# Kernel optimization log

Measured on AMD Instinct MI355X. Metric: run time of the kernel, lower is better.

The kernel has to match this reference:

```python
import jax, jax.numpy as jnp
import numpy as np

DECAY = 0.99
EPS = 1e-05


def setup_inputs() -> dict:
    key = jax.random.key(0)
    k1, k2, k3 = jax.random.split(key, 3)
    inputs = jax.random.normal(k1, (16, 32, 32, 128), dtype=jnp.float32)
    cluster_mean = jax.random.normal(k2, (128, 10000), dtype=jnp.float32)
    cluster_sum = jax.random.normal(k3, (128, 10000), dtype=jnp.float32)
    cluster_size = jnp.zeros((10000,), dtype=jnp.float32)
    return {"inputs": inputs, "cluster_mean": cluster_mean,
            "cluster_sum": cluster_sum, "cluster_size": cluster_size}


def reference(inputs, cluster_mean, cluster_sum, cluster_size):
    embed_dim, n_embed = cluster_mean.shape
    samples = inputs.reshape(-1, embed_dim)                      # [N, E]

    # squared-euclidean distance to each codebook entry: [N, K]
    dist = (jnp.sum(samples ** 2, axis=1, keepdims=True)
            - 2.0 * samples @ cluster_mean
            + jnp.sum(cluster_mean ** 2, axis=0, keepdims=True))
    cluster_index = jnp.argmin(dist, axis=1)                     # [N] int

    # EMA statistics (segment-sum instead of materializing [N, K] one-hot)
    counts = jax.ops.segment_sum(jnp.ones_like(cluster_index, dtype=samples.dtype),
                                 cluster_index, num_segments=n_embed)      # [K]
    sums = jax.ops.segment_sum(samples, cluster_index, num_segments=n_embed).T  # [E, K]

    new_cluster_size = cluster_size * DECAY + counts * (1.0 - DECAY)
    new_cluster_sum = cluster_sum * DECAY + sums * (1.0 - DECAY)

    n_sample = jnp.sum(new_cluster_size)
    smoothed = (new_cluster_size + EPS) * n_sample / (n_sample + n_embed * EPS)
    new_cluster_mean = new_cluster_sum / smoothed                # [E, K]

    idx_grid = cluster_index.reshape(inputs.shape[:-1])          # [B, H, W]
    quantize = new_cluster_mean.T[idx_grid]                      # [B, H, W, E]

    e_loss = jnp.mean((inputs - jax.lax.stop_gradient(quantize)) ** 2)
    outputs = inputs + jax.lax.stop_gradient(quantize - inputs)  # straight-through
    return outputs, 0.25 * e_loss, new_cluster_mean, new_cluster_size, new_cluster_sum
```

## Files before the change

kernel.cpp:

```cpp
#include <hip/hip_runtime.h>

#define NS 16384
#define ED 128
#define KC 10000
#define KP 10240
#define EKTOT (ED*KC)

#define O_OUT  0
#define O_LOSS (NS*ED)
#define O_MEAN (O_LOSS+1)
#define O_SIZE (O_MEAN+EKTOT)
#define O_SUM  (O_SIZE+KC)

#define WB_BEST  0u
#define WB_CNORM 131072u
#define WB_IDX   172032u
#define WB_CNT   237568u
#define WB_NS    278528u
#define WB_XH    294912u
#define WB_XL    4489216u
#define WB_MH    8683520u
#define WB_ML    11304960u

typedef _Float16 f16;
typedef _Float16 f16x8 __attribute__((ext_vector_type(8)));
typedef _Float16 f16x4 __attribute__((ext_vector_type(4)));
typedef float f32x4 __attribute__((ext_vector_type(4)));

constexpr float DECAY = 0.99f;
constexpr float OMD   = 0.01f;
constexpr float EPSV  = 1e-5f;

__global__ void k_prep(const float* __restrict__ X, const float* __restrict__ M,
                       const float* __restrict__ CZ,
                       f16* __restrict__ Xh, f16* __restrict__ Xl,
                       f16* __restrict__ Mh, f16* __restrict__ Ml,
                       float* __restrict__ cnorm, float* __restrict__ cnt,
                       unsigned long long* __restrict__ best,
                       float* __restrict__ out, float* __restrict__ ns_cz) {
    const int b = blockIdx.x, t = threadIdx.x;
    if (b < 2048) {
        int i = (b * 256 + t) * 4;
        float4 v = *(const float4*)(X + i);
        f16x4 h, l;
        h[0] = (f16)v.x; l[0] = (f16)(v.x - (float)h[0]);
        h[1] = (f16)v.y; l[1] = (f16)(v.y - (float)h[1]);
        h[2] = (f16)v.z; l[2] = (f16)(v.z - (float)h[2]);
        h[3] = (f16)v.w; l[3] = (f16)(v.w - (float)h[3]);
        *(f16x4*)(Xh + i) = h;
        *(f16x4*)(Xl + i) = l;
        if (t < 160) {
            int f4 = b * 160 + t;
            if (f4 * 4 < EKTOT) *(float4*)(out + f4 * 4) = make_float4(0.f, 0.f, 0.f, 0.f);
        }
    } else if (b < 2088) {
        int k = (b - 2048) * 256 + t;
        float s = __builtin_inff();
        if (k < KC) {
            s = 0.f;
            #pragma unroll
            for (int c = 0; c < 16; ++c) {
                f16x8 h, l;
                #pragma unroll
                for (int j = 0; j < 8; ++j) {
                    float m = M[(size_t)(c * 8 + j) * KC + k];
                    s = fmaf(m, m, s);
                    h[j] = (f16)m;
                    l[j] = (f16)(m - (float)h[j]);
                }
                *(f16x8*)(Mh + (size_t)k * ED + c * 8) = h;
                *(f16x8*)(Ml + (size_t)k * ED + c * 8) = l;
            }
        } else {
            f16x8 z = {0, 0, 0, 0, 0, 0, 0, 0};
            #pragma unroll
            for (int c = 0; c < 16; ++c) {
                *(f16x8*)(Mh + (size_t)k * ED + c * 8) = z;
                *(f16x8*)(Ml + (size_t)k * ED + c * 8) = z;
            }
        }
        cnorm[k] = s;
        cnt[k] = 0.f;
        for (int i = k; i < NS; i += 40 * 256) best[i] = ~0ull;
    } else {
        __shared__ float red[256];
        float s = 0.f;
        for (int i = t; i < KC; i += 256) s += CZ[i];
        red[t] = s;
        __syncthreads();
        for (int st = 128; st > 0; st >>= 1) {
            if (t < st) red[t] += red[t + st];
            __syncthreads();
        }
        if (t == 0) { *ns_cz = red[0]; out[O_LOSS] = 0.f; }
    }
}

__launch_bounds__(256, 4)
__global__ void k_assign(const f16* __restrict__ Xh, const f16* __restrict__ Xl,
                         const f16* __restrict__ Mh, const f16* __restrict__ Ml,
                         const float* __restrict__ cnorm,
                         unsigned long long* __restrict__ best) {
    __shared__ f16 As[128 * 64];
    __shared__ f16 Bs[128 * 64];

    const int c0 = blockIdx.x * 128;
    const int n0 = blockIdx.y * 128;
    const int t = threadIdx.x, w = t >> 6, l = t & 63;
    const int wr = w >> 1, wc = w & 1;
    const int lg = l >> 4, li = l & 15;

    f32x4 acc[4][4];
    #pragma unroll
    for (int i = 0; i < 4; ++i)
        #pragma unroll
        for (int j = 0; j < 4; ++j) acc[i][j] = (f32x4)0.f;

    const f16* Ap[6] = {Xh, Xh, Xl, Xh, Xh, Xl};
    const f16* Bp[6] = {Mh, Ml, Mh, Mh, Ml, Mh};

    for (int st = 0; st < 6; ++st) {
        const int hh = st < 3 ? 0 : 1;
        const bool loadA = (st != 1) && (st != 4);
        const f16* A = Ap[st];
        const f16* B = Bp[st];
        __syncthreads();
        #pragma unroll
        for (int it = 0; it < 4; ++it) {
            int f = it * 256 + t;
            int row = f >> 3, seg = f & 7;
            int segS = seg ^ (row & 7);
            const f16* gb = B + (size_t)(c0 + row) * ED + hh * 64 + segS * 8;
            f16* lb = Bs + (it * 256 + w * 64) * 8;
            __builtin_amdgcn_global_load_lds(
                (const __attribute__((address_space(1))) unsigned int*)gb,
                (__attribute__((address_space(3))) unsigned int*)lb, 16, 0, 0);
            if (loadA) {
                const f16* ga = A + (size_t)(n0 + row) * ED + hh * 64 + segS * 8;
                f16* la = As + (it * 256 + w * 64) * 8;
                __builtin_amdgcn_global_load_lds(
                    (const __attribute__((address_space(1))) unsigned int*)ga,
                    (__attribute__((address_space(3))) unsigned int*)la, 16, 0, 0);
            }
        }
        __syncthreads();
        #pragma unroll
        for (int ks = 0; ks < 2; ++ks) {
            f16x8 a[4], b[4];
            #pragma unroll
            for (int i = 0; i < 4; ++i) {
                int r = wr * 64 + i * 16 + li;
                a[i] = *(const f16x8*)(As + r * 64 + ((ks * 32 + lg * 8) ^ ((r & 7) << 3)));
            }
            #pragma unroll
            for (int j = 0; j < 4; ++j) {
                int r = wc * 64 + j * 16 + li;
                b[j] = *(const f16x8*)(Bs + r * 64 + ((ks * 32 + lg * 8) ^ ((r & 7) << 3)));
            }
            #pragma unroll
            for (int i = 0; i < 4; ++i)
                #pragma unroll
                for (int j = 0; j < 4; ++j)
                    acc[i][j] = __builtin_amdgcn_mfma_f32_16x16x32_f16(a[i], b[j], acc[i][j], 0, 0, 0);
        }
    }

    float cn[4];
    #pragma unroll
    for (int j = 0; j < 4; ++j) cn[j] = cnorm[c0 + wc * 64 + j * 16 + li];

    #pragma unroll
    for (int i = 0; i < 4; ++i) {
        #pragma unroll
        for (int r = 0; r < 4; ++r) {
            float bv = __builtin_inff(); int bc = 0;
            #pragma unroll
            for (int j = 0; j < 4; ++j) {
                int c = c0 + wc * 64 + j * 16 + li;
                float d = fmaf(-2.f, acc[i][j][r], cn[j]);
                if (d < bv) { bv = d; bc = c; }
            }
            #pragma unroll
            for (int off = 1; off < 16; off <<= 1) {
                float v2 = __shfl_xor(bv, off);
                int   c2 = __shfl_xor(bc, off);
                if (v2 < bv || (v2 == bv && c2 < bc)) { bv = v2; bc = c2; }
            }
            if (li == 0) {
                unsigned u = __float_as_uint(bv);
                u = (u & 0x80000000u) ? ~u : (u | 0x80000000u);
                unsigned long long key = ((unsigned long long)u << 32) | (unsigned)bc;
                atomicMin(best + (n0 + wr * 64 + i * 16 + lg * 4 + r), key);
            }
        }
    }
}

__global__ void k_scatter(const float* __restrict__ X,
                          const unsigned long long* __restrict__ best,
                          int* __restrict__ idx,
                          float* __restrict__ sumT, float* __restrict__ cnt) {
    int tt = blockIdx.x * 256 + threadIdx.x;
    int n = tt >> 7, e = tt & 127;
    int k = (int)(unsigned)(best[n] & 0xFFFFFFFFull);
    if (e == 0) { idx[n] = k; atomicAdd(cnt + k, 1.0f); }
    atomicAdd(sumT + (size_t)k * ED + e, X[tt] * OMD);
}

__global__ void k_mean(const float* __restrict__ csum, const float* __restrict__ csize,
                       const float* __restrict__ cnt, const float* __restrict__ ns_cz,
                       float* __restrict__ out, float* __restrict__ meanT) {
    __shared__ float lds[64 * 129];
    const int k0 = blockIdx.x * 64;
    const int t = threadIdx.x;
    const float* sumT = out;

    #pragma unroll
    for (int r = 0; r < 32; ++r) {
        int f = r * 256 + t;
        int kl = f >> 7, e = f & 127;
        float v = (k0 + kl < KC) ? sumT[(size_t)(k0 + kl) * ED + e] : 0.f;
        lds[kl * 129 + e] = v;
    }
    __syncthreads();

    const int kl2 = t & 63, ww = t >> 6;
    const int k = k0 + kl2;
    if (k < KC) {
        float nsz = fmaf(csize[k], DECAY, cnt[k] * OMD);
        if (ww == 0) out[O_SIZE + k] = nsz;
        float ns  = fmaf(*ns_cz, DECAY, OMD * (float)NS);
        float sm  = (nsz + EPSV) * ns / (ns + (float)KC * EPSV);
        float inv = 1.f / sm;
        #pragma unroll
        for (int r2 = 0; r2 < 32; ++r2) {
            int e2 = r2 * 4 + ww;
            float s   = lds[kl2 * 129 + e2];
            float ncs = fmaf(csum[(size_t)e2 * KC + k], DECAY, s);
            out[O_SUM  + (size_t)e2 * KC + k] = ncs;
            float mean = ncs * inv;
            out[O_MEAN + (size_t)e2 * KC + k] = mean;
            lds[kl2 * 129 + e2] = mean;
        }
    }
    __syncthreads();

    #pragma unroll
    for (int r = 0; r < 32; ++r) {
        int f = r * 256 + t;
        int kl = f >> 7, e = f & 127;
        if (k0 + kl < KC) meanT[(size_t)(k0 + kl) * ED + e] = lds[kl * 129 + e];
    }
}

__global__ void k_gather(const float* __restrict__ X, const int* __restrict__ idx,
                         const float* __restrict__ meanT, float* __restrict__ out) {
    __shared__ float red[256];
    int tt = blockIdx.x * 256 + threadIdx.x;
    int n = tt >> 7, e = tt & 127;
    int k = idx[n];
    float q = meanT[(size_t)k * ED + e];
    float x = X[tt];
    out[O_OUT + tt] = x + (q - x);
    float d = x - q;
    red[threadIdx.x] = d * d;
    __syncthreads();
    for (int s = 128; s > 0; s >>= 1) {
        if (threadIdx.x < s) red[threadIdx.x] += red[threadIdx.x + s];
        __syncthreads();
    }
    if (threadIdx.x == 0)
        atomicAdd(out + O_LOSS, red[0] * (0.25f / (float)(NS * ED)));
}

extern "C" void kernel_launch(void* const* d_in, const int* in_sizes, int n_in,
                              void* d_out, int out_size, void* d_ws, size_t ws_size,
                              hipStream_t stream) {
    const float* X  = (const float*)d_in[0];
    const float* M  = (const float*)d_in[1];
    const float* CS = (const float*)d_in[2];
    const float* CZ = (const float*)d_in[3];
    float* out = (float*)d_out;

    char* wsb = (char*)d_ws;
    unsigned long long* best = (unsigned long long*)(wsb + WB_BEST);
    float* cnorm = (float*)(wsb + WB_CNORM);
    int*   idx   = (int*)(wsb + WB_IDX);
    float* cnt   = (float*)(wsb + WB_CNT);
    float* ns_cz = (float*)(wsb + WB_NS);
    f16* Xh = (f16*)(wsb + WB_XH);
    f16* Xl = (f16*)(wsb + WB_XL);
    f16* Mh = (f16*)(wsb + WB_MH);
    f16* Ml = (f16*)(wsb + WB_ML);
    float* sumT  = out;
    float* meanT = (float*)(wsb + WB_XH);

    hipLaunchKernelGGL(k_prep,   dim3(2089),               dim3(256), 0, stream,
                       X, M, CZ, Xh, Xl, Mh, Ml, cnorm, cnt, best, out, ns_cz);
    hipLaunchKernelGGL(k_assign, dim3(KP / 128, NS / 128), dim3(256), 0, stream,
                       Xh, Xl, Mh, Ml, cnorm, best);
    hipLaunchKernelGGL(k_scatter,dim3(NS * ED / 256),      dim3(256), 0, stream,
                       X, best, idx, sumT, cnt);
    hipLaunchKernelGGL(k_mean,   dim3((KC + 63) / 64),     dim3(256), 0, stream,
                       CS, CZ, cnt, ns_cz, out, meanT);
    hipLaunchKernelGGL(k_gather, dim3(NS * ED / 256),      dim3(256), 0, stream,
                       X, idx, meanT, out);
}
```

Measured before the change: 369.8 us.

## Double-buffer LDS tiles in assignment GEMM with 32-wide K stages

Splits the split-precision distance GEMM's K loop into twelve 32-wide stages and alternates between two LDS buffers. Each iteration issues the global-to-LDS loads for the next stage before running the current stage's MFMAs, so memory latency can overlap with compute. This also drops to one barrier per stage instead of two. The LDS swizzle is reworked for the narrower 32-column rows. Stages that reuse the A tile still skip reloading it, relying on the matching buffer holding the same A slice from two stages earlier.

```diff
diff --git a/kernel.cpp b/kernel.cpp
--- a/kernel.cpp
+++ b/kernel.cpp
@@ -101,11 +101,12 @@
                          const f16* __restrict__ Mh, const f16* __restrict__ Ml,
                          const float* __restrict__ cnorm,
                          unsigned long long* __restrict__ best) {
-    __shared__ f16 As[128 * 64];
-    __shared__ f16 Bs[128 * 64];
+    __shared__ f16 As[2][128 * 32];
+    __shared__ f16 Bs[2][128 * 32];
 
     const int c0 = blockIdx.x * 128;
     const int n0 = blockIdx.y * 128;
+
     const int t = threadIdx.x, w = t >> 6, l = t & 63;
     const int wr = w >> 1, wc = w & 1;
     const int lg = l >> 4, li = l & 15;
@@ -116,53 +117,57 @@
         #pragma unroll
         for (int j = 0; j < 4; ++j) acc[i][j] = (f32x4)0.f;
 
-    const f16* Ap[6] = {Xh, Xh, Xl, Xh, Xh, Xl};
-    const f16* Bp[6] = {Mh, Ml, Mh, Mh, Ml, Mh};
-
-    for (int st = 0; st < 6; ++st) {
-        const int hh = st < 3 ? 0 : 1;
-        const bool loadA = (st != 1) && (st != 4);
-        const f16* A = Ap[st];
-        const f16* B = Bp[st];
-        __syncthreads();
-        #pragma unroll
-        for (int it = 0; it < 4; ++it) {
-            int f = it * 256 + t;
-            int row = f >> 3, seg = f & 7;
-            int segS = seg ^ (row & 7);
-            const f16* gb = B + (size_t)(c0 + row) * ED + hh * 64 + segS * 8;
-            f16* lb = Bs + (it * 256 + w * 64) * 8;
+    auto stageFn = [&](int st, int buf) {
+        const int hh = st / 6, r6 = st % 6, p = r6 >> 1, q = r6 & 1;
+        const f16* A = (p == 2) ? Xl : Xh;
+        const f16* B = (p == 1) ? Ml : Mh;
+        const int kofs = hh * 64 + q * 32;
+        const bool loadA = (p != 1);
+        #pragma unroll
+        for (int it = 0; it < 2; ++it) {
+            int c = it * 256 + t;
+            int row = c >> 2, seg = c & 3;
+            int segS = seg ^ ((row >> 1) & 3);
+            const f16* gb = B + (size_t)(c0 + row) * ED + kofs + segS * 8;
+            f16* lb = &Bs[buf][(it * 256 + w * 64) * 8];
             __builtin_amdgcn_global_load_lds(
                 (const __attribute__((address_space(1))) unsigned int*)gb,
                 (__attribute__((address_space(3))) unsigned int*)lb, 16, 0, 0);
             if (loadA) {
-                const f16* ga = A + (size_t)(n0 + row) * ED + hh * 64 + segS * 8;
-                f16* la = As + (it * 256 + w * 64) * 8;
+                const f16* ga = A + (size_t)(n0 + row) * ED + kofs + segS * 8;
+                f16* la = &As[buf][(it * 256 + w * 64) * 8];
                 __builtin_amdgcn_global_load_lds(
                     (const __attribute__((address_space(1))) unsigned int*)ga,
                     (__attribute__((address_space(3))) unsigned int*)la, 16, 0, 0);
             }
         }
+    };
+
+    stageFn(0, 0);
+    __syncthreads();
+    #pragma unroll
+    for (int st = 0; st < 12; ++st) {
+        const int cur = st & 1;
+        if (st < 11) stageFn(st + 1, cur ^ 1);
+
+        f16x8 a[4], b[4];
+        #pragma unroll
+        for (int i = 0; i < 4; ++i) {
+            int r = wr * 64 + i * 16 + li;
+            a[i] = *(const f16x8*)(&As[cur][r * 32 + ((lg ^ ((r >> 1) & 3)) << 3)]);
+        }
+        #pragma unroll
+        for (int j = 0; j < 4; ++j) {
+            int r = wc * 64 + j * 16 + li;
+            b[j] = *(const f16x8*)(&Bs[cur][r * 32 + ((lg ^ ((r >> 1) & 3)) << 3)]);
+        }
+        #pragma unroll
+        for (int i = 0; i < 4; ++i)
+            #pragma unroll
+            for (int j = 0; j < 4; ++j)
+                acc[i][j] = __builtin_amdgcn_mfma_f32_16x16x32_f16(a[i], b[j], acc[i][j], 0, 0, 0);
+
         __syncthreads();
-        #pragma unroll
-        for (int ks = 0; ks < 2; ++ks) {
-            f16x8 a[4], b[4];
-            #pragma unroll
-            for (int i = 0; i < 4; ++i) {
-                int r = wr * 64 + i * 16 + li;
-                a[i] = *(const f16x8*)(As + r * 64 + ((ks * 32 + lg * 8) ^ ((r & 7) << 3)));
-            }
-            #pragma unroll
-            for (int j = 0; j < 4; ++j) {
-                int r = wc * 64 + j * 16 + li;
-                b[j] = *(const f16x8*)(Bs + r * 64 + ((ks * 32 + lg * 8) ^ ((r & 7) << 3)));
-            }
-            #pragma unroll
-            for (int i = 0; i < 4; ++i)
-                #pragma unroll
-                for (int j = 0; j < 4; ++j)
-                    acc[i][j] = __builtin_amdgcn_mfma_f32_16x16x32_f16(a[i], b[j], acc[i][j], 0, 0, 0);
-        }
     }
 
     float cn[4];
```

After: 374.5 us. Within noise of the previous version (+1.3%).
